# Kernel optimization log

Measured on AMD Instinct MI355X. Metric: run time of the kernel, lower is better.

The kernel has to match this reference:

```python
import math
import jax, jax.numpy as jnp
import numpy as np

B, T, D, H = 2, 2048, 1024, 16
N_LAYERS = 24


def get_slopes(n):
    def pow2(n):
        start = 2 ** (-2 ** (-(math.log2(n) - 3)))
        return [start * start ** i for i in range(n)]
    if math.log2(n).is_integer():
        return pow2(n)
    c = 2 ** math.floor(math.log2(n))
    return pow2(c) + get_slopes(2 * c)[0::2][: n - c]


def setup_inputs() -> dict:
    key = jax.random.key(0)
    ks = jax.random.split(key, 5)
    x = jax.random.normal(ks[0], (B, T, D), dtype=jnp.float32)
    Wq = 0.02 * jax.random.normal(ks[1], (D, D), dtype=jnp.float32)
    Wk = 0.02 * jax.random.normal(ks[2], (D, D), dtype=jnp.float32)
    Wv = 0.02 * jax.random.normal(ks[3], (D, D), dtype=jnp.float32)
    Wo = (0.02 / math.sqrt(2 * N_LAYERS)) * jax.random.normal(ks[4], (D, D), dtype=jnp.float32)
    z = jnp.zeros((D,), dtype=jnp.float32)
    return {"x": x, "Wq": Wq, "bq": z, "Wk": Wk, "bk": z, "Wv": Wv, "bv": z, "Wo": Wo, "bo": z}


def reference(x, Wq, bq, Wk, bk, Wv, bv, Wo, bo):
    Bb, Tt, C = x.shape
    hd = C // H
    # QKV projections -> (B, H, T, hd)
    q = (x @ Wq + bq).reshape(Bb, Tt, H, hd).transpose(0, 2, 1, 3)
    k = (x @ Wk + bk).reshape(Bb, Tt, H, hd).transpose(0, 2, 1, 3)
    v = (x @ Wv + bv).reshape(Bb, Tt, H, hd).transpose(0, 2, 1, 3)
    # scaled dot-product scores (B, H, T, T)
    attn = jnp.einsum('bhqd,bhkd->bhqk', q, k) / jnp.sqrt(jnp.asarray(hd, x.dtype))
    # ALiBi bias: module uses only last row of the relative-position matrix,
    # broadcast over query positions: -slope_h * (T-1 - j), shape (1, H, 1, T)
    slopes = jnp.asarray(get_slopes(H), dtype=x.dtype)
    alibi = -slopes[None, :, None, None] * (Tt - 1 - jnp.arange(Tt, dtype=x.dtype))[None, None, None, :]
    attn = attn + alibi
    # causal mask
    causal = jnp.tril(jnp.ones((Tt, Tt), dtype=bool))[None, None, :, :]
    attn = jnp.where(causal, attn, jnp.finfo(x.dtype).min)
    p = jax.nn.softmax(attn, axis=-1)
    out = jnp.einsum('bhqk,bhkd->bqhd', p, v).reshape(Bb, Tt, C)
    return out @ Wo + bo
```

## Files before the change

### kernel.cpp

```cpp
#include <hip/hip_runtime.h>
#include <hip/hip_bf16.h>

#define Bn 2
#define Tdim 2048
#define Ddim 1024
#define Hn 16
#define HD 64

typedef unsigned short u16;
typedef unsigned int u32;
typedef __attribute__((ext_vector_type(8))) __bf16 bf16x8;
typedef __attribute__((ext_vector_type(4))) float f32x4;
typedef __attribute__((ext_vector_type(16))) float f32x16;
typedef __attribute__((ext_vector_type(4))) u32 u32x4;

struct alignas(8) U16x4 { u16 x, y, z, w; };

__device__ __forceinline__ u16 f2bf(float f) {
  union { float f; u32 i; } v; v.f = f;
  u32 x = v.i;
  u32 r = (x + 0x7fffu + ((x >> 16) & 1u)) >> 16;
  return (u16)r;
}
__device__ __forceinline__ float bf2f(u16 u) {
  union { u32 i; float f; } v; v.i = ((u32)u) << 16; return v.f;
}

__device__ __forceinline__ u32 cvtpk_bf16(float a, float b) {
  u32 d;
  asm("v_cvt_pk_bf16_f32 %0, %1, %2" : "=v"(d) : "v"(a), "v"(b));
  return d;
}

__device__ __forceinline__ void cp16(const u16* g, u16* l) {
  __builtin_amdgcn_global_load_lds(
      (const __attribute__((address_space(1))) u32*)g,
      (__attribute__((address_space(3))) u32*)l, 16, 0, 0);
}

__device__ __forceinline__ f32x4 mfma16(bf16x8 a, bf16x8 b, f32x4 c) {
  return __builtin_amdgcn_mfma_f32_16x16x32_bf16(a, b, c, 0, 0, 0);
}
__device__ __forceinline__ f32x16 mfma32(bf16x8 a, bf16x8 b, f32x16 c) {
  return __builtin_amdgcn_mfma_f32_32x32x16_bf16(a, b, c, 0, 0, 0);
}

__global__ __launch_bounds__(256) void convert_x(const float* __restrict__ src,
                                                 u16* __restrict__ dst) {
  const int i = (blockIdx.x * 256 + threadIdx.x) * 8;
  u16 t[8];
#pragma unroll
  for (int j = 0; j < 8; j++) t[j] = f2bf(src[i + j]);
  *(bf16x8*)&dst[i] = *(const bf16x8*)t;
}

__global__ __launch_bounds__(256) void transpose_k(
    const float* __restrict__ s0, const float* __restrict__ s1,
    const float* __restrict__ s2, const float* __restrict__ s3,
    u16* __restrict__ dst) {
  const float* src = (blockIdx.z == 0) ? s0 : (blockIdx.z == 1) ? s1
                   : (blockIdx.z == 2) ? s2 : s3;
  u16* d = dst + (size_t)blockIdx.z * Ddim * Ddim;
  __shared__ u16 tile[32][33];
  const int tx = threadIdx.x, ty = threadIdx.y;
  const int x = blockIdx.x * 32 + tx;
  const int y0 = blockIdx.y * 32;
#pragma unroll
  for (int j = 0; j < 32; j += 8) tile[ty + j][tx] = f2bf(src[(size_t)(y0 + ty + j) * Ddim + x]);
  __syncthreads();
  const int xo = blockIdx.y * 32 + tx;
  const int yo0 = blockIdx.x * 32;
#pragma unroll
  for (int j = 0; j < 32; j += 8) d[(size_t)(yo0 + ty + j) * Ddim + xo] = tile[tx][ty + j];
}

__global__ __launch_bounds__(256, 2) void gemm_qkv(
    const u16* __restrict__ Xb, const u16* __restrict__ WT,
    const float* __restrict__ bq, const float* __restrict__ bk, const float* __restrict__ bv,
    u16* __restrict__ Q, u16* __restrict__ K, u16* __restrict__ Vt) {
  const int flat = blockIdx.x + 32 * (blockIdx.y + 8 * blockIdx.z);
  const int l = (flat & 7) * 96 + (flat >> 3);
  const int lbx = l & 31, lby = (l >> 5) & 7, z = l >> 8;

  const u16* Wt = WT + (size_t)z * Ddim * Ddim;
  const float* bias = (z == 0) ? bq : (z == 1) ? bk : bv;
  u16* QK = (z == 0) ? Q : K;

  __shared__ alignas(16) u16 Alds[128 * 32];
  __shared__ alignas(16) u16 Blds[128 * 32];
  const int tid = threadIdx.x;
  const int w = tid >> 6, lane = tid & 63, ln = lane & 15, quad = lane >> 4;
  const int wm = (w >> 1) * 64, wn = (w & 1) * 64;
  const int tm = lbx * 128, tn = lby * 128;

  f32x4 acc[4][4] = {};

  const int srow = tid >> 2, scol = (tid & 3) * 8;
  const u16* ag = Xb + (size_t)(tm + srow) * Ddim + scol;
  const u16* ag2 = ag + (size_t)64 * Ddim;
  const u16* bg = Wt + (size_t)(tn + srow) * Ddim + scol;
  const u16* bg2 = bg + (size_t)64 * Ddim;
  u16* al = &Alds[w * 512];
  u16* al2 = &Alds[2048 + w * 512];
  u16* bl = &Blds[w * 512];
  u16* bl2 = &Blds[2048 + w * 512];

  for (int k0 = 0; k0 < Ddim; k0 += 32) {
    __syncthreads();
    cp16(ag + k0, al);
    cp16(ag2 + k0, al2);
    cp16(bg + k0, bl);
    cp16(bg2 + k0, bl2);
    __syncthreads();
    bf16x8 af[4], bfr[4];
#pragma unroll
    for (int i = 0; i < 4; i++)
      af[i] = *(const bf16x8*)&Alds[(wm + i * 16 + ln) * 32 + quad * 8];
#pragma unroll
    for (int i = 0; i < 4; i++)
      bfr[i] = *(const bf16x8*)&Blds[(wn + i * 16 + ln) * 32 + quad * 8];
#pragma unroll
    for (int mi = 0; mi < 4; mi++)
#pragma unroll
      for (int ni = 0; ni < 4; ni++)
        acc[mi][ni] = mfma16(af[mi], bfr[ni], acc[mi][ni]);
  }

#pragma unroll
  for (int mi = 0; mi < 4; mi++) {
#pragma unroll
    for (int ni = 0; ni < 4; ni++) {
      const int gm0 = tm + wm + mi * 16 + quad * 4;
      const int gn = tn + wn + ni * 16 + ln;
      const float bv_ = bias[gn];
      const int hh = gn >> 6, dd = gn & 63;
      const int b0 = gm0 >> 11, t0 = gm0 & 2047;
      if (z < 2) {
        u16* p = QK + (((size_t)(b0 * Hn + hh) * Tdim) + t0) * HD + dd;
#pragma unroll
        for (int r = 0; r < 4; r++) p[r * HD] = f2bf(acc[mi][ni][r] + bv_);
      } else {
        U16x4 pk;
        pk.x = f2bf(acc[mi][ni][0] + bv_);
        pk.y = f2bf(acc[mi][ni][1] + bv_);
        pk.z = f2bf(acc[mi][ni][2] + bv_);
        pk.w = f2bf(acc[mi][ni][3] + bv_);
        *(U16x4*)&Vt[((size_t)(b0 * Hn + hh) * HD + dd) * Tdim + t0] = pk;
      }
    }
  }
}

#define KSTR 68
#define VSTR 132
#define L2E 1.44269504088896f
__global__ __launch_bounds__(256, 2) void attn_k(
    const u16* __restrict__ Q, const u16* __restrict__ K, const u16* __restrict__ Vt,
    u16* __restrict__ Op, float* __restrict__ lp) {
  __shared__ alignas(16) u16 Klds[128 * KSTR];
  __shared__ alignas(16) u16 Vtlds[64 * VSTR];

  const int id = blockIdx.x;
  const int xcd = id & 7, slot = id >> 3;
  const int bh = (xcd << 2) | (slot >> 4);
  const int inner = slot & 15;
  const int p = inner >> 1;
  const int s = inner & 1;
  const int tid = threadIdx.x;
  const int w = tid >> 6, lane = tid & 63;
  const int qi = lane & 31, hf = lane >> 5;

  const u16* Qh = Q + (size_t)bh * Tdim * HD;
  const u16* Kh = K + (size_t)bh * Tdim * HD;
  const u16* Vh = Vt + (size_t)bh * HD * Tdim;
  const float slope = exp2f(-0.5f * (float)((bh & 15) + 1));

  const float sl2 = slope * L2E;
  const float c1 = 0.125f * L2E;
  const float f4hf = (float)(4 * hf);
  float sg8[4], slm[4];
#pragma unroll
  for (int g = 0; g < 4; g++) sg8[g] = sl2 * (float)(8 * g);
#pragma unroll
  for (int m = 0; m < 4; m++) slm[m] = sl2 * (float)m;

  const int qbs[2] = {p, 15 - p};
  int K0[2], K1[2];
#pragma unroll
  for (int seg = 0; seg < 2; seg++) {
    const int nk = qbs[seg] + 1;
    const int h0 = (nk + 1) >> 1;
    K0[seg] = s ? h0 : 0;
    K1[seg] = s ? nk : h0;
  }

  bf16x8 kreg[4], vreg[4];
  {
    const int kb = ((K0[0] < K1[0]) ? K0[0] : K0[1]) * 128;
#pragma unroll
    for (int c = 0; c < 4; c++) {
      const int e = c * 2048 + tid * 8;
      kreg[c] = *(const bf16x8*)&Kh[(size_t)(kb + (e >> 6)) * HD + (e & 63)];
      vreg[c] = *(const bf16x8*)&Vh[(size_t)(e >> 7) * Tdim + kb + (e & 127)];
    }
  }

  for (int seg = 0; seg < 2; seg++) {
    const int qb = qbs[seg];
    const int kt0 = K0[seg], kt1 = K1[seg];
    const int nkt = qb + 1;
    const int q0 = qb * 128;
    const int tg = q0 + w * 32 + qi;
    const float tt2 = (slope * (float)tg + 3.0f) * L2E;

    bf16x8 qf[4];
#pragma unroll
    for (int kc = 0; kc < 4; kc++)
      qf[kc] = *(const bf16x8*)&Qh[(size_t)tg * HD + kc * 16 + hf * 8];

    float ls0 = 0.f, ls1 = 0.f;
    f32x16 oacc[2] = {};

    for (int kt = kt0; kt < kt1; kt++) {
      const int kb = kt * 128;
      __syncthreads();
#pragma unroll
      for (int c = 0; c < 4; c++) {
        const int e = c * 2048 + tid * 8;
        *(bf16x8*)&Klds[(e >> 6) * KSTR + (e & 63)] = kreg[c];
        *(bf16x8*)&Vtlds[(e >> 7) * VSTR + (e & 127)] = vreg[c];
      }
      __syncthreads();

      {
        const int nxt = (kt + 1 < kt1) ? (kt + 1) : ((seg == 0) ? K0[1] : -1);
        if (nxt >= 0) {
          const int kb2 = nxt * 128;
#pragma unroll
          for (int c = 0; c < 4; c++) {
            const int e = c * 2048 + tid * 8;
            kreg[c] = *(const bf16x8*)&Kh[(size_t)(kb2 + (e >> 6)) * HD + (e & 63)];
            vreg[c] = *(const bf16x8*)&Vh[(size_t)(e >> 7) * Tdim + kb2 + (e & 127)];
          }
        }
      }

      f32x16 st[4] = {};
      __builtin_amdgcn_s_setprio(1);
#pragma unroll
      for (int kc = 0; kc < 4; kc++) {
#pragma unroll
        for (int ni = 0; ni < 4; ni++) {
          bf16x8 kf = *(const bf16x8*)&Klds[(ni * 32 + qi) * KSTR + kc * 16 + hf * 8];
          st[ni] = mfma32(kf, qf[kc], st[ni]);
        }
      }
      __builtin_amdgcn_s_setprio(0);

      const bool diag = (kt == nkt - 1);
      const float fkb = (float)kb + f4hf;
      bf16x8 pfrag[8];
#pragma unroll
      for (int ni = 0; ni < 4; ni++) {
        const float cni = __builtin_fmaf(sl2, fkb + (float)(32 * ni), -tt2);
        float pv[16];
        if (!diag) {
#pragma unroll
          for (int ri = 0; ri < 16; ri++) {
            const float e = __builtin_fmaf(st[ni][ri], c1, cni + sg8[ri >> 2] + slm[ri & 3]);
            const float pp = __builtin_amdgcn_exp2f(e);
            if (ri & 1) ls1 += pp; else ls0 += pp;
            pv[ri] = pp;
          }
        } else {
#pragma unroll
          for (int ri = 0; ri < 16; ri++) {
            const int n = kb + ni * 32 + (ri & 3) + 8 * (ri >> 2) + 4 * hf;
            const float e = __builtin_fmaf(st[ni][ri], c1, cni + sg8[ri >> 2] + slm[ri & 3]);
            float pp = __builtin_amdgcn_exp2f(e);
            if (n > tg) pp = 0.f;
            if (ri & 1) ls1 += pp; else ls0 += pp;
            pv[ri] = pp;
          }
        }
        u32 pk[4][2];
#pragma unroll
        for (int g = 0; g < 4; g++) {
          pk[g][0] = cvtpk_bf16(pv[g * 4 + 0], pv[g * 4 + 1]);
          pk[g][1] = cvtpk_bf16(pv[g * 4 + 2], pv[g * 4 + 3]);
        }
#pragma unroll
        for (int a = 0; a < 2; a++) {
          const u32 snd0 = (hf == 0) ? pk[2 * a + 1][0] : pk[2 * a][0];
          const u32 snd1 = (hf == 0) ? pk[2 * a + 1][1] : pk[2 * a][1];
          const u32 rcv0 = (u32)__shfl_xor((int)snd0, 32);
          const u32 rcv1 = (u32)__shfl_xor((int)snd1, 32);
          u32x4 fr;
          fr.x = (hf == 0) ? pk[2 * a][0] : rcv0;
          fr.y = (hf == 0) ? pk[2 * a][1] : rcv1;
          fr.z = (hf == 0) ? rcv0 : pk[2 * a + 1][0];
          fr.w = (hf == 0) ? rcv1 : pk[2 * a + 1][1];
          pfrag[ni * 2 + a] = *(bf16x8*)&fr;
        }
      }

      __builtin_amdgcn_s_setprio(1);
#pragma unroll
      for (int kf16 = 0; kf16 < 8; kf16++) {
#pragma unroll
        for (int nd = 0; nd < 2; nd++) {
          bf16x8 vf = *(const bf16x8*)&Vtlds[(nd * 32 + qi) * VSTR + kf16 * 16 + hf * 8];
          oacc[nd] = mfma32(pfrag[kf16], vf, oacc[nd]);
        }
      }
      __builtin_amdgcn_s_setprio(0);
    }

    float lsum = ls0 + ls1;
    lsum += __shfl_xor(lsum, 32);
    if (hf == 0) lp[(size_t)s * 65536 + bh * Tdim + tg] = lsum;

    u16* Ob = Op + (size_t)s * (32u * Tdim * HD) + ((size_t)bh * Tdim) * HD;
#pragma unroll
    for (int nd = 0; nd < 2; nd++) {
#pragma unroll
      for (int ri = 0; ri < 16; ri++) {
        const int rq = (ri & 3) + 8 * (ri >> 2) + 4 * hf;
        const int t = q0 + w * 32 + rq;
        Ob[(size_t)t * HD + nd * 32 + qi] = f2bf(oacc[nd][ri]);
      }
    }
  }
}

__global__ __launch_bounds__(256) void merge_k(const u16* __restrict__ Op,
                                               const float* __restrict__ lp,
                                               u16* __restrict__ AO) {
  const int i = blockIdx.x * 256 + threadIdx.x;
  const int d8 = i & 7;
  const int t = (i >> 3) & 2047;
  const int bh = i >> 14;
  const int b = bh >> 4, h = bh & 15;
  const float l = lp[bh * Tdim + t] + lp[65536 + bh * Tdim + t];
  const float inv = 1.0f / l;
  const size_t off = ((size_t)bh * Tdim + t) * HD + d8 * 8;
  const u16* O0 = Op + off;
  const u16* O1 = Op + (size_t)32 * Tdim * HD + off;
  u16 outv[8];
#pragma unroll
  for (int j = 0; j < 8; j++)
    outv[j] = f2bf((bf2f(O0[j]) + bf2f(O1[j])) * inv);
  *(bf16x8*)&AO[((size_t)(b * Tdim + t)) * Ddim + h * HD + d8 * 8] = *(const bf16x8*)outv;
}

__global__ __launch_bounds__(256, 2) void gemm_out(
    const u16* __restrict__ A, const u16* __restrict__ WoT, const float* __restrict__ bo,
    float* __restrict__ C) {
  const int flat = blockIdx.x + 64 * blockIdx.y;
  const int l = (flat & 7) * 64 + (flat >> 3);
  const int lbx = l & 63, lby = l >> 6;

  __shared__ alignas(16) u16 Alds[64 * 32];
  __shared__ alignas(16) u16 Blds[128 * 32];
  const int tid = threadIdx.x;
  const int w = tid >> 6, lane = tid & 63, ln = lane & 15, quad = lane >> 4;
  const int tm = lbx * 64, tn = lby * 128;

  f32x4 acc[4][2] = {};

  const int srow = tid >> 2, scol = (tid & 3) * 8;
  const u16* ag = A + (size_t)(tm + srow) * Ddim + scol;
  const u16* bg = WoT + (size_t)(tn + srow) * Ddim + scol;
  const u16* bg2 = bg + (size_t)64 * Ddim;
  u16* al = &Alds[w * 512];
  u16* bl = &Blds[w * 512];
  u16* bl2 = &Blds[2048 + w * 512];

  for (int k0 = 0; k0 < Ddim; k0 += 32) {
    __syncthreads();
    cp16(ag + k0, al);
    cp16(bg + k0, bl);
    cp16(bg2 + k0, bl2);
    __syncthreads();
    bf16x8 af[4], bfr[2];
#pragma unroll
    for (int i = 0; i < 4; i++)
      af[i] = *(const bf16x8*)&Alds[(i * 16 + ln) * 32 + quad * 8];
#pragma unroll
    for (int i = 0; i < 2; i++)
      bfr[i] = *(const bf16x8*)&Blds[(w * 32 + i * 16 + ln) * 32 + quad * 8];
#pragma unroll
    for (int mi = 0; mi < 4; mi++)
#pragma unroll
      for (int ni = 0; ni < 2; ni++)
        acc[mi][ni] = mfma16(af[mi], bfr[ni], acc[mi][ni]);
  }

#pragma unroll
  for (int mi = 0; mi < 4; mi++) {
#pragma unroll
    for (int ni = 0; ni < 2; ni++) {
      const int gm0 = tm + mi * 16 + quad * 4;
      const int gn = tn + w * 32 + ni * 16 + ln;
      const float bv_ = bo[gn];
#pragma unroll
      for (int r = 0; r < 4; r++)
        C[(size_t)(gm0 + r) * Ddim + gn] = acc[mi][ni][r] + bv_;
    }
  }
}

extern "C" void kernel_launch(void* const* d_in, const int* in_sizes, int n_in,
                              void* d_out, int out_size, void* d_ws, size_t ws_size,
                              hipStream_t stream) {
  (void)in_sizes; (void)n_in; (void)out_size; (void)ws_size;
  const float* x  = (const float*)d_in[0];
  const float* Wq = (const float*)d_in[1];
  const float* bq = (const float*)d_in[2];
  const float* Wk = (const float*)d_in[3];
  const float* bk = (const float*)d_in[4];
  const float* Wv = (const float*)d_in[5];
  const float* bv = (const float*)d_in[6];
  const float* Wo = (const float*)d_in[7];
  const float* bo = (const float*)d_in[8];

  char* ws = (char*)d_ws;
  const size_t MB = 1024 * 1024;
  u16* WT   = (u16*)(ws + 0 * MB);
  u16* Qb   = (u16*)(ws + 8 * MB);
  u16* Kb   = (u16*)(ws + 16 * MB);
  u16* Vtb  = (u16*)(ws + 24 * MB);
  u16* Xb   = (u16*)(ws + 32 * MB);
  u16* AO   = (u16*)(ws + 32 * MB);
  u16* Opart= (u16*)(ws + 40 * MB);
  float* lpart = (float*)(ws + 56 * MB);
  u16* WoT = WT + (size_t)3 * Ddim * Ddim;

  convert_x<<<dim3(2048), 256, 0, stream>>>(x, Xb);
  transpose_k<<<dim3(32, 32, 4), dim3(32, 8), 0, stream>>>(Wq, Wk, Wv, Wo, WT);

  gemm_qkv<<<dim3(32, 8, 3), 256, 0, stream>>>(Xb, WT, bq, bk, bv, Qb, Kb, Vtb);
  attn_k<<<dim3(512), 256, 0, stream>>>(Qb, Kb, Vtb, Opart, lpart);
  merge_k<<<dim3(2048), 256, 0, stream>>>(Opart, lpart, AO);
  gemm_out<<<dim3(64, 8), 256, 0, stream>>>(AO, WoT, bo, (float*)d_out);
}
```

Measured before the change: 184.4 us.

## Double GEMM K-tile to 64 with XOR-swizzled LDS layout

Both the QKV and output-projection GEMMs now stage 64-wide K slices per iteration instead of 32, halving the number of barrier pairs per K loop. The LDS layout uses an XOR swizzle on 16-byte chunks (column chunk XOR row) so that the wider rows do not cause bank conflicts on the fragment reads. The cost is doubled shared-memory use per block, which may reduce occupancy, and global loads are now issued per wave in 8-row groups.

New measurement: 182.7 us. Within noise of the previous version (-0.9%).

```diff
diff --git a/kernel.cpp b/kernel.cpp
--- a/kernel.cpp
+++ b/kernel.cpp
@@ -86,8 +86,8 @@
   const float* bias = (z == 0) ? bq : (z == 1) ? bk : bv;
   u16* QK = (z == 0) ? Q : K;
 
-  __shared__ alignas(16) u16 Alds[128 * 32];
-  __shared__ alignas(16) u16 Blds[128 * 32];
+  __shared__ alignas(16) u16 Alds[128 * 64];
+  __shared__ alignas(16) u16 Blds[128 * 64];
   const int tid = threadIdx.x;
   const int w = tid >> 6, lane = tid & 63, ln = lane & 15, quad = lane >> 4;
   const int wm = (w >> 1) * 64, wn = (w & 1) * 64;
@@ -95,35 +95,35 @@
 
   f32x4 acc[4][4] = {};
 
-  const int srow = tid >> 2, scol = (tid & 3) * 8;
-  const u16* ag = Xb + (size_t)(tm + srow) * Ddim + scol;
-  const u16* ag2 = ag + (size_t)64 * Ddim;
-  const u16* bg = Wt + (size_t)(tn + srow) * Ddim + scol;
-  const u16* bg2 = bg + (size_t)64 * Ddim;
-  u16* al = &Alds[w * 512];
-  u16* al2 = &Alds[2048 + w * 512];
-  u16* bl = &Blds[w * 512];
-  u16* bl2 = &Blds[2048 + w * 512];
-
-  for (int k0 = 0; k0 < Ddim; k0 += 32) {
+  const int srow = lane >> 3;
+  const int scol = ((lane & 7) ^ srow) * 8;
+  const u16* ag0 = Xb + (size_t)(tm + w * 32 + srow) * Ddim + scol;
+  const u16* bg0 = Wt + (size_t)(tn + w * 32 + srow) * Ddim + scol;
+
+  for (int k0 = 0; k0 < Ddim; k0 += 64) {
     __syncthreads();
-    cp16(ag + k0, al);
-    cp16(ag2 + k0, al2);
-    cp16(bg + k0, bl);
-    cp16(bg2 + k0, bl2);
+#pragma unroll
+    for (int j = 0; j < 4; j++) {
+      cp16(ag0 + (size_t)j * 8 * Ddim + k0, &Alds[(w * 32 + j * 8) * 64]);
+      cp16(bg0 + (size_t)j * 8 * Ddim + k0, &Blds[(w * 32 + j * 8) * 64]);
+    }
     __syncthreads();
-    bf16x8 af[4], bfr[4];
-#pragma unroll
-    for (int i = 0; i < 4; i++)
-      af[i] = *(const bf16x8*)&Alds[(wm + i * 16 + ln) * 32 + quad * 8];
-#pragma unroll
-    for (int i = 0; i < 4; i++)
-      bfr[i] = *(const bf16x8*)&Blds[(wn + i * 16 + ln) * 32 + quad * 8];
-#pragma unroll
-    for (int mi = 0; mi < 4; mi++)
-#pragma unroll
-      for (int ni = 0; ni < 4; ni++)
-        acc[mi][ni] = mfma16(af[mi], bfr[ni], acc[mi][ni]);
+#pragma unroll
+    for (int k2 = 0; k2 < 2; k2++) {
+      const int so = ((k2 * 4 + quad) ^ (ln & 7)) * 8;
+      bf16x8 af[4], bfr[4];
+#pragma unroll
+      for (int i = 0; i < 4; i++)
+        af[i] = *(const bf16x8*)&Alds[(wm + i * 16 + ln) * 64 + so];
+#pragma unroll
+      for (int i = 0; i < 4; i++)
+        bfr[i] = *(const bf16x8*)&Blds[(wn + i * 16 + ln) * 64 + so];
+#pragma unroll
+      for (int mi = 0; mi < 4; mi++)
+#pragma unroll
+        for (int ni = 0; ni < 4; ni++)
+          acc[mi][ni] = mfma16(af[mi], bfr[ni], acc[mi][ni]);
+    }
   }
 
 #pragma unroll
@@ -360,40 +360,44 @@
   const int l = (flat & 7) * 64 + (flat >> 3);
   const int lbx = l & 63, lby = l >> 6;
 
-  __shared__ alignas(16) u16 Alds[64 * 32];
-  __shared__ alignas(16) u16 Blds[128 * 32];
+  __shared__ alignas(16) u16 Alds[64 * 64];
+  __shared__ alignas(16) u16 Blds[128 * 64];
   const int tid = threadIdx.x;
   const int w = tid >> 6, lane = tid & 63, ln = lane & 15, quad = lane >> 4;
   const int tm = lbx * 64, tn = lby * 128;
 
   f32x4 acc[4][2] = {};
 
-  const int srow = tid >> 2, scol = (tid & 3) * 8;
-  const u16* ag = A + (size_t)(tm + srow) * Ddim + scol;
-  const u16* bg = WoT + (size_t)(tn + srow) * Ddim + scol;
-  const u16* bg2 = bg + (size_t)64 * Ddim;
-  u16* al = &Alds[w * 512];
-  u16* bl = &Blds[w * 512];
-  u16* bl2 = &Blds[2048 + w * 512];
-
-  for (int k0 = 0; k0 < Ddim; k0 += 32) {
+  const int srow = lane >> 3;
+  const int scol = ((lane & 7) ^ srow) * 8;
+  const u16* ag0 = A + (size_t)(tm + w * 16 + srow) * Ddim + scol;
+  const u16* bg0 = WoT + (size_t)(tn + w * 32 + srow) * Ddim + scol;
+
+  for (int k0 = 0; k0 < Ddim; k0 += 64) {
     __syncthreads();
-    cp16(ag + k0, al);
-    cp16(bg + k0, bl);
-    cp16(bg2 + k0, bl2);
+#pragma unroll
+    for (int j = 0; j < 2; j++)
+      cp16(ag0 + (size_t)j * 8 * Ddim + k0, &Alds[(w * 16 + j * 8) * 64]);
+#pragma unroll
+    for (int j = 0; j < 4; j++)
+      cp16(bg0 + (size_t)j * 8 * Ddim + k0, &Blds[(w * 32 + j * 8) * 64]);
     __syncthreads();
-    bf16x8 af[4], bfr[2];
-#pragma unroll
-    for (int i = 0; i < 4; i++)
-      af[i] = *(const bf16x8*)&Alds[(i * 16 + ln) * 32 + quad * 8];
-#pragma unroll
-    for (int i = 0; i < 2; i++)
-      bfr[i] = *(const bf16x8*)&Blds[(w * 32 + i * 16 + ln) * 32 + quad * 8];
-#pragma unroll
-    for (int mi = 0; mi < 4; mi++)
-#pragma unroll
-      for (int ni = 0; ni < 2; ni++)
-        acc[mi][ni] = mfma16(af[mi], bfr[ni], acc[mi][ni]);
+#pragma unroll
+    for (int k2 = 0; k2 < 2; k2++) {
+      const int so = ((k2 * 4 + quad) ^ (ln & 7)) * 8;
+      bf16x8 af[4], bfr[2];
+#pragma unroll
+      for (int i = 0; i < 4; i++)
+        af[i] = *(const bf16x8*)&Alds[(i * 16 + ln) * 64 + so];
+#pragma unroll
+      for (int i = 0; i < 2; i++)
+        bfr[i] = *(const bf16x8*)&Blds[(w * 32 + i * 16 + ln) * 64 + so];
+#pragma unroll
+      for (int mi = 0; mi < 4; mi++)
+#pragma unroll
+        for (int ni = 0; ni < 2; ni++)
+          acc[mi][ni] = mfma16(af[mi], bfr[ni], acc[mi][ni]);
+    }
   }
 
 #pragma unroll
```
